# Performance work log

Hardware: AMD Instinct MI355X
Metric: run time of the kernel (lower is better)

The kernel has to match this reference:

```python
import jax, jax.numpy as jnp
import numpy as np

N_HEAD = 16
N_KV_HEAD = 4
HEAD_DIM = 64
VE_CH = 12  # min(12, n_embd)


def apply_rotary_emb(x, cos, sin):
    d = x.shape[3] // 2
    x1, x2 = x[..., :d], x[..., d:]
    return jnp.concatenate([x1 * cos + x2 * sin, x1 * -sin + x2 * cos], axis=3)


def rms_norm(x):
    return x * jax.lax.rsqrt(jnp.mean(jnp.square(x), axis=-1, keepdims=True) + 1e-6)


def setup_inputs() -> dict:
    key = jax.random.key(0)
    ks = jax.random.split(key, 9)
    B, T, C = 2, 2048, 1024
    s = 0.02
    return {
        "x": jax.random.normal(ks[0], (B, T, C), jnp.float32),
        "ve": jax.random.normal(ks[1], (B, T, N_KV_HEAD * HEAD_DIM), jnp.float32),
        "cos": jax.random.normal(ks[2], (1, T, 1, HEAD_DIM // 2), jnp.float32),
        "sin": jax.random.normal(ks[3], (1, T, 1, HEAD_DIM // 2), jnp.float32),
        "Wq": jax.random.normal(ks[4], (C, C), jnp.float32) * s,
        "Wk": jax.random.normal(ks[5], (N_KV_HEAD * HEAD_DIM, C), jnp.float32) * s,
        "Wv": jax.random.normal(ks[6], (N_KV_HEAD * HEAD_DIM, C), jnp.float32) * s,
        "Wo": jax.random.normal(ks[7], (C, C), jnp.float32) * s,
        "Wg": jax.random.normal(ks[8], (N_KV_HEAD, VE_CH), jnp.float32) * s,
    }


def reference(x, ve, cos, sin, Wq, Wk, Wv, Wo, Wg):
    B, T, C = x.shape
    q = (x @ Wq.T).reshape(B, T, N_HEAD, HEAD_DIM)
    k = (x @ Wk.T).reshape(B, T, N_KV_HEAD, HEAD_DIM)
    v = (x @ Wv.T).reshape(B, T, N_KV_HEAD, HEAD_DIM)

    # value-embedding gate
    ve_r = ve.reshape(B, T, N_KV_HEAD, HEAD_DIM)
    gate = 3.0 * jax.nn.sigmoid(x[..., :VE_CH] @ Wg.T)  # [B,T,n_kv_head]
    v = v + gate[..., None] * ve_r

    q = apply_rotary_emb(q, cos, sin)
    k = apply_rotary_emb(k, cos, sin)
    q = rms_norm(q) * 1.2
    k = rms_norm(k) * 1.2

    # GQA: expand kv heads
    r = N_HEAD // N_KV_HEAD
    k = jnp.repeat(k, r, axis=2)
    v = jnp.repeat(v, r, axis=2)

    # [B,H,T,D]
    q = q.transpose(0, 2, 1, 3)
    k = k.transpose(0, 2, 1, 3)
    v = v.transpose(0, 2, 1, 3)

    scale = 1.0 / np.sqrt(HEAD_DIM).astype(np.float32)
    scores = jnp.einsum("bhqd,bhkd->bhqk", q, k) * scale
    causal = jnp.tril(jnp.ones((T, T), dtype=bool))
    scores = jnp.where(causal, scores, jnp.float32(-jnp.inf))
    att = jax.nn.softmax(scores, axis=-1)
    y = jnp.einsum("bhqk,bhkd->bhqd", att, v)
    y = y.transpose(0, 2, 1, 3).reshape(B, T, C)
    return y @ Wo.T
```

## Files before the change

### kernel.cpp

```cpp
#include <hip/hip_runtime.h>
#include <stdint.h>

#define B_SZ 2
#define T_SZ 2048
#define C_SZ 1024
#define NH   16
#define NKV  4
#define HD   64
#define KVD  256
#define QKV_N 1536

typedef __attribute__((ext_vector_type(8))) short bf16x8;
typedef __attribute__((ext_vector_type(4))) float f32x4;

#define GL(p) ((const __attribute__((address_space(1))) void*)(p))
#define LD(p) ((__attribute__((address_space(3))) void*)(p))

__device__ inline unsigned short f2bf(float f) {
  union { float f; unsigned u; } v; v.f = f;
  unsigned u = v.u;
  unsigned r = (u + 0x7fffu + ((u >> 16) & 1u)) >> 16;
  return (unsigned short)r;
}
__device__ inline unsigned short bftrunc(float f) {
  union { float f; unsigned u; } v; v.f = f;
  return (unsigned short)(v.u >> 16);
}

struct CvtArgs {
  const float *s0, *s1, *s2, *s3, *s4;
  unsigned short *d0, *d1, *d2, *d3, *d4;
  const float *x, *Wg;
  float *gate;
};
__global__ __launch_bounds__(256) void cvt_all(CvtArgs a) {
  int blk = blockIdx.x, tid = threadIdx.x;
  if (blk >= 6656) {
    int idx = (blk - 6656) * 256 + tid;
    int bt = idx >> 2, kh = idx & 3;
    float s = 0.f;
#pragma unroll
    for (int j = 0; j < 12; j++) s += a.x[(size_t)bt * C_SZ + j] * a.Wg[kh * 12 + j];
    a.gate[idx] = 3.f / (1.f + __expf(-s));
    return;
  }
  const float* s; unsigned short* d; int i;
  if      (blk < 4096) { s = a.s0; d = a.d0; i = blk * 256 + tid; }
  else if (blk < 5120) { s = a.s1; d = a.d1; i = (blk - 4096) * 256 + tid; }
  else if (blk < 5376) { s = a.s2; d = a.d2; i = (blk - 5120) * 256 + tid; }
  else if (blk < 5632) { s = a.s3; d = a.d3; i = (blk - 5376) * 256 + tid; }
  else                 { s = a.s4; d = a.d4; i = (blk - 5632) * 256 + tid; }
  float4 f = ((const float4*)s)[i];
  ushort4 o;
  o.x = f2bf(f.x); o.y = f2bf(f.y); o.z = f2bf(f.z); o.w = f2bf(f.w);
  ((ushort4*)d)[i] = o;
}

#define GEMM_PROLOG(A, Bm, K)                                                        \
  __shared__ unsigned short As[2][64 * 64];                                          \
  __shared__ unsigned short Bs[2][128 * 64];                                         \
  int tid  = threadIdx.x;                                                            \
  int lane = tid & 63;                                                               \
  int wave = tid >> 6;                                                               \
  int quad = lane >> 4;                                                              \
  int l16  = lane & 15;                                                              \
  int m0 = blockIdx.y * 64;                                                          \
  int n0 = blockIdx.x * 128;                                                         \
  int wm = (wave & 1) * 32;                                                          \
  int wn = (wave >> 1) * 64;                                                         \
  f32x4 acc[2][4];                                                                   \
  _Pragma("unroll") for (int i = 0; i < 2; i++)                                      \
    _Pragma("unroll") for (int j = 0; j < 4; j++)                                    \
      acc[i][j] = (f32x4){0.f, 0.f, 0.f, 0.f};                                       \
  int lrow = lane >> 3;                                 \
  int lcol = ((lane & 7) ^ lrow) * 8;                 \
  int sA = wave * 16;                                                                \
  int sB = wave * 32;                                                                \
  const unsigned short* aP0 = &A[(size_t)(m0 + sA + lrow) * K + lcol];               \
  const unsigned short* aP1 = aP0 + 8 * (size_t)K;                                   \
  const unsigned short* bP0 = &Bm[(size_t)(n0 + sB + lrow) * K + lcol];              \
  const unsigned short* bP1 = bP0 + 8 * (size_t)K;                                   \
  const unsigned short* bP2 = bP0 + 16 * (size_t)K;                                  \
  const unsigned short* bP3 = bP0 + 24 * (size_t)K;                                  \
  __builtin_amdgcn_global_load_lds(GL(aP0), LD(&As[0][(sA     ) * 64]), 16, 0, 0);   \
  __builtin_amdgcn_global_load_lds(GL(aP1), LD(&As[0][(sA +  8) * 64]), 16, 0, 0);   \
  __builtin_amdgcn_global_load_lds(GL(bP0), LD(&Bs[0][(sB     ) * 64]), 16, 0, 0);   \
  __builtin_amdgcn_global_load_lds(GL(bP1), LD(&Bs[0][(sB +  8) * 64]), 16, 0, 0);   \
  __builtin_amdgcn_global_load_lds(GL(bP2), LD(&Bs[0][(sB + 16) * 64]), 16, 0, 0);   \
  __builtin_amdgcn_global_load_lds(GL(bP3), LD(&Bs[0][(sB + 24) * 64]), 16, 0, 0);   \
  int swz = l16 & 7;                                                                 \
  int nk = K >> 6;                                                                   \
  for (int ki = 0; ki < nk; ki++) {                                                  \
    int cur = ki & 1, nxt = cur ^ 1;                                                 \
    __syncthreads();                                                                 \
    if (ki + 1 < nk) {                                                               \
      int k0 = (ki + 1) << 6;                                                        \
      __builtin_amdgcn_global_load_lds(GL(aP0 + k0), LD(&As[nxt][(sA     ) * 64]), 16, 0, 0); \
      __builtin_amdgcn_global_load_lds(GL(aP1 + k0), LD(&As[nxt][(sA +  8) * 64]), 16, 0, 0); \
      __builtin_amdgcn_global_load_lds(GL(bP0 + k0), LD(&Bs[nxt][(sB     ) * 64]), 16, 0, 0); \
      __builtin_amdgcn_global_load_lds(GL(bP1 + k0), LD(&Bs[nxt][(sB +  8) * 64]), 16, 0, 0); \
      __builtin_amdgcn_global_load_lds(GL(bP2 + k0), LD(&Bs[nxt][(sB + 16) * 64]), 16, 0, 0); \
      __builtin_amdgcn_global_load_lds(GL(bP3 + k0), LD(&Bs[nxt][(sB + 24) * 64]), 16, 0, 0); \
    }                                                                                \
    _Pragma("unroll") for (int p = 0; p < 2; p++) {                                  \
      bf16x8 af[2], bfr[4];                                                          \
      _Pragma("unroll") for (int i = 0; i < 2; i++)                                  \
        af[i] = *(const bf16x8*)&As[cur][(wm + i * 16 + l16) * 64 + (((p * 4 + quad) ^ swz) * 8)]; \
      _Pragma("unroll") for (int j = 0; j < 4; j++)                                  \
        bfr[j] = *(const bf16x8*)&Bs[cur][(wn + j * 16 + l16) * 64 + (((p * 4 + quad) ^ swz) * 8)]; \
      _Pragma("unroll") for (int i = 0; i < 2; i++)                                  \
        _Pragma("unroll") for (int j = 0; j < 4; j++)                                \
          acc[i][j] = __builtin_amdgcn_mfma_f32_16x16x32_bf16(af[i], bfr[j], acc[i][j], 0, 0, 0); \
    }                                                                                \
  }

__global__ __launch_bounds__(256) void gemm_bt(const unsigned short* __restrict__ A,
                                               const unsigned short* __restrict__ Bm,
                                               float* __restrict__ C,
                                               int N, int K) {
  GEMM_PROLOG(A, Bm, K)
#pragma unroll
  for (int i = 0; i < 2; i++) {
#pragma unroll
    for (int j = 0; j < 4; j++) {
      int col = n0 + wn + j * 16 + l16;
#pragma unroll
      for (int r = 0; r < 4; r++) {
        int row = m0 + wm + i * 16 + quad * 4 + r;
        C[(size_t)row * N + col] = acc[i][j][r];
      }
    }
  }
}

__global__ __launch_bounds__(256) void gemm_qkv(const unsigned short* __restrict__ A,
                                                const unsigned short* __restrict__ Bm,
                                                const float* __restrict__ ve,
                                                const float* __restrict__ cosb,
                                                const float* __restrict__ sinb,
                                                const float* __restrict__ gateArr,
                                                unsigned short* __restrict__ qa,
                                                unsigned short* __restrict__ ka,
                                                unsigned short* __restrict__ vtmp) {
  const int K = C_SZ;
  GEMM_PROLOG(A, Bm, K)

  int colbase = n0 + wn;
  if (colbase < 1280) {
    int isQ = colbase < 1024;
    int h   = isQ ? (colbase >> 6) : ((colbase - 1024) >> 6);
    float scale = isQ ? (0.15f * 1.44269504088896f) : 1.2f;
    unsigned short* dst = isQ ? qa : ka;
    int nheads = isQ ? NH : NKV;
#pragma unroll
    for (int i = 0; i < 2; i++) {
#pragma unroll
      for (int r = 0; r < 4; r++) {
        int row = m0 + wm + i * 16 + quad * 4 + r;
        int t = row & (T_SZ - 1), b = row >> 11;
        float a10 = acc[i][0][r], a11 = acc[i][1][r];
        float a20 = acc[i][2][r], a21 = acc[i][3][r];
        float cv0 = cosb[t * 32 + l16],      sv0 = sinb[t * 32 + l16];
        float cv1 = cosb[t * 32 + 16 + l16], sv1 = sinb[t * 32 + 16 + l16];
        float o10 =  a10 * cv0 + a20 * sv0;
        float o11 =  a11 * cv1 + a21 * sv1;
        float o20 = -a10 * sv0 + a20 * cv0;
        float o21 = -a11 * sv1 + a21 * cv1;
        float ssq = o10 * o10 + o11 * o11 + o20 * o20 + o21 * o21;
        ssq += __shfl_xor(ssq, 1);
        ssq += __shfl_xor(ssq, 2);
        ssq += __shfl_xor(ssq, 4);
        ssq += __shfl_xor(ssq, 8);
        float rn = rsqrtf(ssq * (1.f / 64.f) + 1e-6f) * scale;
        size_t base = ((size_t)(b * nheads + h) * T_SZ + t) * HD;
        dst[base + l16]      = f2bf(o10 * rn);
        dst[base + 16 + l16] = f2bf(o11 * rn);
        dst[base + 32 + l16] = f2bf(o20 * rn);
        dst[base + 48 + l16] = f2bf(o21 * rn);
      }
    }
  } else {
    int kh = (colbase - 1280) >> 6;
#pragma unroll
    for (int i = 0; i < 2; i++) {
#pragma unroll
      for (int r = 0; r < 4; r++) {
        int row = m0 + wm + i * 16 + quad * 4 + r;
        float g = gateArr[row * 4 + kh];
#pragma unroll
        for (int j = 0; j < 4; j++) {
          int d = j * 16 + l16;
          float val = acc[i][j][r] + g * ve[(size_t)row * KVD + kh * HD + d];
          vtmp[(size_t)row * KVD + kh * HD + d] = f2bf(val);
        }
      }
    }
  }
}

__global__ __launch_bounds__(256) void v_transpose(const unsigned short* __restrict__ vtmp,
                                                   unsigned short* __restrict__ vt) {
  __shared__ unsigned short tile[64 * 68];
  int blk = blockIdx.x;
  int tb = blk & 31, kh = (blk >> 5) & 3, b = blk >> 7;
  int tid = threadIdx.x;
  int r = tid >> 2, c = (tid & 3) * 16;
  const unsigned short* src = &vtmp[((size_t)(b * T_SZ + tb * 64 + r)) * KVD + kh * HD + c];
  uint4 x0 = *(const uint4*)(src);
  uint4 x1 = *(const uint4*)(src + 8);
  *(uint2*)&tile[r * 68 + c]      = *(uint2*)&x0;
  *(uint2*)&tile[r * 68 + c + 4]  = *((uint2*)&x0 + 1);
  *(uint2*)&tile[r * 68 + c + 8]  = *(uint2*)&x1;
  *(uint2*)&tile[r * 68 + c + 12] = *((uint2*)&x1 + 1);
  __syncthreads();
  int d = tid >> 2, tc = (tid & 3) * 16;
  ushort4 o0, o1, o2, o3;
  o0.x = tile[(tc + 0) * 68 + d];  o0.y = tile[(tc + 1) * 68 + d];
  o0.z = tile[(tc + 2) * 68 + d];  o0.w = tile[(tc + 3) * 68 + d];
  o1.x = tile[(tc + 4) * 68 + d];  o1.y = tile[(tc + 5) * 68 + d];
  o1.z = tile[(tc + 6) * 68 + d];  o1.w = tile[(tc + 7) * 68 + d];
  o2.x = tile[(tc + 8) * 68 + d];  o2.y = tile[(tc + 9) * 68 + d];
  o2.z = tile[(tc + 10) * 68 + d]; o2.w = tile[(tc + 11) * 68 + d];
  o3.x = tile[(tc + 12) * 68 + d]; o3.y = tile[(tc + 13) * 68 + d];
  o3.z = tile[(tc + 14) * 68 + d]; o3.w = tile[(tc + 15) * 68 + d];
  unsigned short* dst = &vt[((size_t)(b * NKV + kh) * HD + d) * T_SZ + tb * 64 + tc];
  *(ushort4*)(dst)      = o0;
  *(ushort4*)(dst + 4)  = o1;
  *(ushort4*)(dst + 8)  = o2;
  *(ushort4*)(dst + 12) = o3;
}

__global__ __launch_bounds__(512, 6) void attn(const unsigned short* __restrict__ qa,
                                               const unsigned short* __restrict__ ka,
                                               const unsigned short* __restrict__ vt,
                                               unsigned short* __restrict__ y) {
  int bid = blockIdx.x;
  int half = bid >> 8, r = bid & 255;
  int qt = half ? (r & 15) : 15 - (r & 15);
  int bh = (half << 4) | (r >> 4);
  int b = bh >> 4, h = bh & 15;
  int kh = h >> 2;
  int tid = threadIdx.x;
  int wave = tid >> 6, lane = tid & 63;
  int quad = lane >> 4, l16 = lane & 15;
  int swz = l16 & 7;

  __shared__ unsigned short Ks[2][64 * 64];
  __shared__ unsigned short Vs[2][64 * 64];
  __shared__ unsigned short Ps[128 * 64];
  unsigned short* Pw = &Ps[(wave * 16) * 64];

  int qrow0 = qt * 128 + wave * 16;

  bf16x8 bq0, bq1;
  {
    int tq = qrow0 + l16;
    const unsigned short* qp = &qa[((size_t)(b * NH + h) * T_SZ + tq) * HD];
    bq0 = *(const bf16x8*)&qp[quad * 8];
    bq1 = *(const bf16x8*)&qp[32 + quad * 8];
  }

  const unsigned short one_bf = 0x3F80;
  bf16x8 vones = {(short)one_bf, (short)one_bf, (short)one_bf, (short)one_bf,
                  (short)one_bf, (short)one_bf, (short)one_bf, (short)one_bf};

  f32x4 oacc[4];
  f32x4 lacc = (f32x4){0.f, 0.f, 0.f, 0.f};
#pragma unroll
  for (int d = 0; d < 4; d++) oacc[d] = (f32x4){0.f, 0.f, 0.f, 0.f};

  int lr  = tid >> 3;
  int lcc = tid & 7;
  int gcol = lcc * 8;
  int soff = lr * 64 + ((lcc ^ (lr & 7)) * 8);

  const unsigned short* kbase = &ka[(size_t)(b * NKV + kh) * T_SZ * HD];
  const unsigned short* vbase = &vt[(size_t)(b * NKV + kh) * HD * T_SZ];

  int nj = 2 * qt + 2;

  {
    uint4 k0 = *(const uint4*)&kbase[(size_t)lr * HD + gcol];
    uint4 v0 = *(const uint4*)&vbase[(size_t)lr * T_SZ + gcol];
    *(uint4*)&Ks[0][soff] = k0;
    *(uint4*)&Vs[0][soff] = v0;
  }

  for (int j = 0; j < nj; j++) {
    int cur = j & 1, nxt = cur ^ 1;
    __syncthreads();

    uint4 k0, v0;
    bool pf = (j + 1 < nj);
    if (pf) {
      k0 = *(const uint4*)&kbase[(size_t)((j + 1) * 64 + lr) * HD + gcol];
      v0 = *(const uint4*)&vbase[(size_t)lr * T_SZ + (j + 1) * 64 + gcol];
    }

    bool active = (j * 64) <= (qrow0 + 15);

    if (active) {
      f32x4 st[4];
#pragma unroll
      for (int tb = 0; tb < 4; tb++) {
        bf16x8 ak0 = *(const bf16x8*)&Ks[cur][(tb * 16 + l16) * 64 + ((quad ^ swz) * 8)];
        bf16x8 ak1 = *(const bf16x8*)&Ks[cur][(tb * 16 + l16) * 64 + (((4 + quad) ^ swz) * 8)];
        f32x4 s = (f32x4){0.f, 0.f, 0.f, 0.f};
        s = __builtin_amdgcn_mfma_f32_16x16x32_bf16(ak0, bq0, s, 0, 0, 0);
        s = __builtin_amdgcn_mfma_f32_16x16x32_bf16(ak1, bq1, s, 0, 0, 0);
        st[tb] = s;
      }

      if (j * 64 + 63 > qrow0) {
        int qg = qrow0 + l16;
#pragma unroll
        for (int tb = 0; tb < 4; tb++) {
          int tg = j * 64 + tb * 16 + quad * 4;
#pragma unroll
          for (int i = 0; i < 4; i++) {
            if (tg + i > qg) st[tb][i] = -__builtin_inff();
          }
        }
      }
#pragma unroll
      for (int tb = 0; tb < 4; tb++) {
        ushort4 w;
        w.x = bftrunc(__builtin_amdgcn_exp2f(st[tb][0]));
        w.y = bftrunc(__builtin_amdgcn_exp2f(st[tb][1]));
        w.z = bftrunc(__builtin_amdgcn_exp2f(st[tb][2]));
        w.w = bftrunc(__builtin_amdgcn_exp2f(st[tb][3]));
        *(ushort4*)&Pw[l16 * 64 + (((tb * 2 + (quad >> 1)) ^ swz) * 8) + (quad & 1) * 4] = w;
      }

      bf16x8 ap0 = *(const bf16x8*)&Pw[l16 * 64 + ((quad ^ swz) * 8)];
      bf16x8 ap1 = *(const bf16x8*)&Pw[l16 * 64 + (((4 + quad) ^ swz) * 8)];
      lacc = __builtin_amdgcn_mfma_f32_16x16x32_bf16(ap0, vones, lacc, 0, 0, 0);
      lacc = __builtin_amdgcn_mfma_f32_16x16x32_bf16(ap1, vones, lacc, 0, 0, 0);
#pragma unroll
      for (int d = 0; d < 4; d++) {
        bf16x8 bv0 = *(const bf16x8*)&Vs[cur][(d * 16 + l16) * 64 + ((quad ^ swz) * 8)];
        bf16x8 bv1 = *(const bf16x8*)&Vs[cur][(d * 16 + l16) * 64 + (((4 + quad) ^ swz) * 8)];
        oacc[d] = __builtin_amdgcn_mfma_f32_16x16x32_bf16(ap0, bv0, oacc[d], 0, 0, 0);
        oacc[d] = __builtin_amdgcn_mfma_f32_16x16x32_bf16(ap1, bv1, oacc[d], 0, 0, 0);
      }
    }

    if (pf) {
      *(uint4*)&Ks[nxt][soff] = k0;
      *(uint4*)&Vs[nxt][soff] = v0;
    }
  }

#pragma unroll
  for (int i = 0; i < 4; i++) {
    int tq = qrow0 + quad * 4 + i;
    float inv = 1.f / lacc[i];
#pragma unroll
    for (int d = 0; d < 4; d++) {
      y[((size_t)(b * T_SZ) + tq) * C_SZ + h * HD + d * 16 + l16] = f2bf(oacc[d][i] * inv);
    }
  }
}

extern "C" void kernel_launch(void* const* d_in, const int* in_sizes, int n_in,
                              void* d_out, int out_size, void* d_ws, size_t ws_size,
                              hipStream_t stream) {
  const float* x    = (const float*)d_in[0];
  const float* ve   = (const float*)d_in[1];
  const float* cosb = (const float*)d_in[2];
  const float* sinb = (const float*)d_in[3];
  const float* Wq   = (const float*)d_in[4];
  const float* Wk   = (const float*)d_in[5];
  const float* Wv   = (const float*)d_in[6];
  const float* Wo   = (const float*)d_in[7];
  const float* Wg   = (const float*)d_in[8];
  float* out = (float*)d_out;

  const size_t MB = 1024 * 1024;
  char* ws = (char*)d_ws;
  unsigned short* xb    = (unsigned short*)(ws);
  unsigned short* wqkvb = (unsigned short*)(ws + 8 * MB);
  unsigned short* wob   = (unsigned short*)(ws + 11 * MB);
  unsigned short* qab   = (unsigned short*)(ws + 13 * MB);
  unsigned short* kab   = (unsigned short*)(ws + 21 * MB);
  unsigned short* vtb   = (unsigned short*)(ws + 23 * MB);
  float*          gateA = (float*)(ws + 25 * MB);
  unsigned short* vtmp  = (unsigned short*)(ws + 26 * MB);
  unsigned short* yb    = xb;

  CvtArgs ca;
  ca.s0 = x;  ca.d0 = xb;
  ca.s1 = Wq; ca.d1 = wqkvb;
  ca.s2 = Wk; ca.d2 = wqkvb + 1024 * 1024;
  ca.s3 = Wv; ca.d3 = wqkvb + 1280 * 1024;
  ca.s4 = Wo; ca.d4 = wob;
  ca.x = x; ca.Wg = Wg; ca.gate = gateA;
  cvt_all<<<6720, 256, 0, stream>>>(ca);

  gemm_qkv<<<dim3(QKV_N / 128, (B_SZ * T_SZ) / 64), 256, 0, stream>>>(
      xb, wqkvb, ve, cosb, sinb, gateA, qab, kab, vtmp);

  v_transpose<<<256, 256, 0, stream>>>(vtmp, vtb);

  attn<<<512, 512, 0, stream>>>(qab, kab, vtb, yb);

  gemm_bt<<<dim3(C_SZ / 128, (B_SZ * T_SZ) / 64), 256, 0, stream>>>(
      yb, wob, out, C_SZ, C_SZ);
}
```

Measured before the change: 164.2 us.

## Load K/V MFMA fragments directly from global memory instead of LDS staging

The attention kernel drops the double-buffered shared-memory K and V tiles and has each wave read its MFMA operand fragments straight from global memory, relying on L1/L2 for reuse across the 8 waves. This removes the LDS staging writes and reads and shrinks shared memory to just the P buffer. The launch-bounds occupancy hint is lowered from 6 to 4, giving the compiler more registers for the extra fragment loads. The trade-off is 8x redundant global/L2 traffic per block, no explicit software prefetch, and stride-heavy fragment loads with higher latency that may stall the MFMA pipeline.

```diff
diff --git a/kernel.cpp b/kernel.cpp
--- a/kernel.cpp
+++ b/kernel.cpp
@@ -230,7 +230,7 @@
   *(ushort4*)(dst + 12) = o3;
 }
 
-__global__ __launch_bounds__(512, 6) void attn(const unsigned short* __restrict__ qa,
+__global__ __launch_bounds__(512, 4) void attn(const unsigned short* __restrict__ qa,
                                                const unsigned short* __restrict__ ka,
                                                const unsigned short* __restrict__ vt,
                                                unsigned short* __restrict__ y) {
@@ -245,8 +245,6 @@
   int quad = lane >> 4, l16 = lane & 15;
   int swz = l16 & 7;
 
-  __shared__ unsigned short Ks[2][64 * 64];
-  __shared__ unsigned short Vs[2][64 * 64];
   __shared__ unsigned short Ps[128 * 64];
   unsigned short* Pw = &Ps[(wave * 16) * 64];
 
@@ -269,85 +267,68 @@
 #pragma unroll
   for (int d = 0; d < 4; d++) oacc[d] = (f32x4){0.f, 0.f, 0.f, 0.f};
 
-  int lr  = tid >> 3;
-  int lcc = tid & 7;
-  int gcol = lcc * 8;
-  int soff = lr * 64 + ((lcc ^ (lr & 7)) * 8);
-
-  const unsigned short* kbase = &ka[(size_t)(b * NKV + kh) * T_SZ * HD];
-  const unsigned short* vbase = &vt[(size_t)(b * NKV + kh) * HD * T_SZ];
+  const unsigned short* kfrag = &ka[(size_t)(b * NKV + kh) * T_SZ * HD + (size_t)l16 * HD + quad * 8];
+  const unsigned short* vfrag = &vt[(size_t)(b * NKV + kh) * HD * T_SZ + (size_t)l16 * T_SZ + quad * 8];
 
   int nj = 2 * qt + 2;
 
-  {
-    uint4 k0 = *(const uint4*)&kbase[(size_t)lr * HD + gcol];
-    uint4 v0 = *(const uint4*)&vbase[(size_t)lr * T_SZ + gcol];
-    *(uint4*)&Ks[0][soff] = k0;
-    *(uint4*)&Vs[0][soff] = v0;
-  }
-
   for (int j = 0; j < nj; j++) {
-    int cur = j & 1, nxt = cur ^ 1;
-    __syncthreads();
-
-    uint4 k0, v0;
-    bool pf = (j + 1 < nj);
-    if (pf) {
-      k0 = *(const uint4*)&kbase[(size_t)((j + 1) * 64 + lr) * HD + gcol];
-      v0 = *(const uint4*)&vbase[(size_t)lr * T_SZ + (j + 1) * 64 + gcol];
-    }
+    __builtin_amdgcn_s_barrier();
 
     bool active = (j * 64) <= (qrow0 + 15);
-
-    if (active) {
-      f32x4 st[4];
+    if (!active) continue;
+
+    int t0 = j * 64;
+
+    f32x4 st[4];
+#pragma unroll
+    for (int tb = 0; tb < 4; tb++) {
+      const unsigned short* kr = kfrag + (size_t)(t0 + tb * 16) * HD;
+      bf16x8 ak0 = *(const bf16x8*)kr;
+      bf16x8 ak1 = *(const bf16x8*)(kr + 32);
+      f32x4 s = (f32x4){0.f, 0.f, 0.f, 0.f};
+      s = __builtin_amdgcn_mfma_f32_16x16x32_bf16(ak0, bq0, s, 0, 0, 0);
+      s = __builtin_amdgcn_mfma_f32_16x16x32_bf16(ak1, bq1, s, 0, 0, 0);
+      st[tb] = s;
+    }
+
+    bf16x8 vf0[4], vf1[4];
+#pragma unroll
+    for (int d = 0; d < 4; d++) {
+      const unsigned short* vr = vfrag + (size_t)(d * 16) * T_SZ + t0;
+      vf0[d] = *(const bf16x8*)vr;
+      vf1[d] = *(const bf16x8*)(vr + 32);
+    }
+
+    if (t0 + 63 > qrow0) {
+      int qg = qrow0 + l16;
 #pragma unroll
       for (int tb = 0; tb < 4; tb++) {
-        bf16x8 ak0 = *(const bf16x8*)&Ks[cur][(tb * 16 + l16) * 64 + ((quad ^ swz) * 8)];
-        bf16x8 ak1 = *(const bf16x8*)&Ks[cur][(tb * 16 + l16) * 64 + (((4 + quad) ^ swz) * 8)];
-        f32x4 s = (f32x4){0.f, 0.f, 0.f, 0.f};
-        s = __builtin_amdgcn_mfma_f32_16x16x32_bf16(ak0, bq0, s, 0, 0, 0);
-        s = __builtin_amdgcn_mfma_f32_16x16x32_bf16(ak1, bq1, s, 0, 0, 0);
-        st[tb] = s;
-      }
-
-      if (j * 64 + 63 > qrow0) {
-        int qg = qrow0 + l16;
-#pragma unroll
-        for (int tb = 0; tb < 4; tb++) {
-          int tg = j * 64 + tb * 16 + quad * 4;
-#pragma unroll
-          for (int i = 0; i < 4; i++) {
-            if (tg + i > qg) st[tb][i] = -__builtin_inff();
-          }
+        int tg = t0 + tb * 16 + quad * 4;
+#pragma unroll
+        for (int i = 0; i < 4; i++) {
+          if (tg + i > qg) st[tb][i] = -__builtin_inff();
         }
       }
-#pragma unroll
-      for (int tb = 0; tb < 4; tb++) {
-        ushort4 w;
-        w.x = bftrunc(__builtin_amdgcn_exp2f(st[tb][0]));
-        w.y = bftrunc(__builtin_amdgcn_exp2f(st[tb][1]));
-        w.z = bftrunc(__builtin_amdgcn_exp2f(st[tb][2]));
-        w.w = bftrunc(__builtin_amdgcn_exp2f(st[tb][3]));
-        *(ushort4*)&Pw[l16 * 64 + (((tb * 2 + (quad >> 1)) ^ swz) * 8) + (quad & 1) * 4] = w;
-      }
-
-      bf16x8 ap0 = *(const bf16x8*)&Pw[l16 * 64 + ((quad ^ swz) * 8)];
-      bf16x8 ap1 = *(const bf16x8*)&Pw[l16 * 64 + (((4 + quad) ^ swz) * 8)];
-      lacc = __builtin_amdgcn_mfma_f32_16x16x32_bf16(ap0, vones, lacc, 0, 0, 0);
-      lacc = __builtin_amdgcn_mfma_f32_16x16x32_bf16(ap1, vones, lacc, 0, 0, 0);
-#pragma unroll
-      for (int d = 0; d < 4; d++) {
-        bf16x8 bv0 = *(const bf16x8*)&Vs[cur][(d * 16 + l16) * 64 + ((quad ^ swz) * 8)];
-        bf16x8 bv1 = *(const bf16x8*)&Vs[cur][(d * 16 + l16) * 64 + (((4 + quad) ^ swz) * 8)];
-        oacc[d] = __builtin_amdgcn_mfma_f32_16x16x32_bf16(ap0, bv0, oacc[d], 0, 0, 0);
-        oacc[d] = __builtin_amdgcn_mfma_f32_16x16x32_bf16(ap1, bv1, oacc[d], 0, 0, 0);
-      }
-    }
-
-    if (pf) {
-      *(uint4*)&Ks[nxt][soff] = k0;
-      *(uint4*)&Vs[nxt][soff] = v0;
+    }
+#pragma unroll
+    for (int tb = 0; tb < 4; tb++) {
+      ushort4 w;
+      w.x = bftrunc(__builtin_amdgcn_exp2f(st[tb][0]));
+      w.y = bftrunc(__builtin_amdgcn_exp2f(st[tb][1]));
+      w.z = bftrunc(__builtin_amdgcn_exp2f(st[tb][2]));
+      w.w = bftrunc(__builtin_amdgcn_exp2f(st[tb][3]));
+      *(ushort4*)&Pw[l16 * 64 + (((tb * 2 + (quad >> 1)) ^ swz) * 8) + (quad & 1) * 4] = w;
+    }
+
+    bf16x8 ap0 = *(const bf16x8*)&Pw[l16 * 64 + ((quad ^ swz) * 8)];
+    bf16x8 ap1 = *(const bf16x8*)&Pw[l16 * 64 + (((4 + quad) ^ swz) * 8)];
+    lacc = __builtin_amdgcn_mfma_f32_16x16x32_bf16(ap0, vones, lacc, 0, 0, 0);
+    lacc = __builtin_amdgcn_mfma_f32_16x16x32_bf16(ap1, vones, lacc, 0, 0, 0);
+#pragma unroll
+    for (int d = 0; d < 4; d++) {
+      oacc[d] = __builtin_amdgcn_mfma_f32_16x16x32_bf16(ap0, vf0[d], oacc[d], 0, 0, 0);
+      oacc[d] = __builtin_amdgcn_mfma_f32_16x16x32_bf16(ap1, vf1[d], oacc[d], 0, 0, 0);
     }
   }
 
```

Measured after the change: 259.7 us. 1.58x slower.
